# Performance work log

Hardware: AMD Instinct MI355X
Metric: run time of the kernel (lower is better)

Reference implementation:

```python
import jax, jax.numpy as jnp
import numpy as np

B, S, F, D, M = 2, 512, 16384, 768, 262144  # batch, seq, n_features, d_model, n_connections


def setup_inputs() -> dict:
    key = jax.random.key(0)
    k1, k2, k3, k4, k5 = jax.random.split(key, 5)
    up_facts = jax.random.normal(k1, (B, S, F), dtype=jnp.float32)
    down_encoder = jax.random.normal(k2, (F, D), dtype=jnp.float32) * 0.02
    up_decoder = jax.random.normal(k3, (D, F), dtype=jnp.float32) * 0.02
    i_indices = jnp.sort(jax.random.randint(k4, (M,), 0, F, dtype=jnp.int32)).astype(jnp.int64)
    j_indices = jax.random.randint(k5, (M,), 0, F, dtype=jnp.int32).astype(jnp.int64)
    return {
        "up_facts": up_facts,
        "down_encoder": down_encoder,
        "up_decoder": up_decoder,
        "i_indices": i_indices,
        "j_indices": j_indices,
    }


def reference(up_facts, down_encoder, up_decoder, i_indices, j_indices):
    # Virtual weight value for each sparse connection (i -> j):
    #   values[m] = <down_encoder[i_m, :], up_decoder[:, j_m]>
    values = jnp.sum(down_encoder[i_indices] * up_decoder[:, j_indices].T, axis=1)  # [M]
    # Gather upstream feature activations for each connection, scale by value.
    scaled = up_facts[:, :, j_indices] * values  # [B, S, M]
    # Scatter-add into downstream feature slots (duplicate i indices accumulate).
    contributions = jnp.zeros((up_facts.shape[0], up_facts.shape[1], down_encoder.shape[0]),
                              dtype=up_facts.dtype)
    return contributions.at[:, :, i_indices].add(scaled)  # [B, S, F]
```

## Files before the change

kernel.cpp:

```cpp
#include <hip/hip_runtime.h>
#include <hip/hip_bf16.h>

#define D_DIM 768
#define F_DIM 16384
#define M_CONN 262144
#define N_ROWS 1024

typedef float f32x4 __attribute__((ext_vector_type(4)));
typedef float f32x2 __attribute__((ext_vector_type(2)));

__device__ __forceinline__ float bf2f(unsigned short u) {
    return __uint_as_float(((unsigned int)u) << 16);
}

__global__ __launch_bounds__(512) void transpose_f32_t(const float* __restrict__ in,
                                                       float* __restrict__ out,
                                                       int R, int C) {
    __shared__ float ldsT[128][132];
    const int t = threadIdx.x;
    const int x0 = blockIdx.x * 128;
    const int y0 = blockIdx.y * 128;
#pragma unroll
    for (int it = 0; it < 8; ++it) {
        const int idx = it * 512 + t;
        const int r = idx >> 5;
        const int c4 = idx & 31;
        const f32x4 v = __builtin_nontemporal_load(
            (const f32x4*)(in + (size_t)(y0 + r) * C + x0 + c4 * 4));
        ldsT[c4 * 4 + 0][r] = v.x;
        ldsT[c4 * 4 + 1][r] = v.y;
        ldsT[c4 * 4 + 2][r] = v.z;
        ldsT[c4 * 4 + 3][r] = v.w;
    }
    __syncthreads();
#pragma unroll
    for (int it = 0; it < 8; ++it) {
        const int idx = it * 512 + t;
        const int c = idx >> 5;
        const int r4 = idx & 31;
        const f32x4 o = *(const f32x4*)&ldsT[c][r4 * 4];
        __builtin_nontemporal_store(
            o, (f32x4*)(out + (size_t)(x0 + c) * R + y0 + r4 * 4));
    }
}

__global__ __launch_bounds__(512) void transpose_f2b_t(const float* __restrict__ in,
                                                       unsigned short* __restrict__ out,
                                                       int R, int C) {
    __shared__ unsigned short ldsT[128][260];
    const int t = threadIdx.x;
    const int x0 = blockIdx.x * 128;
    const int y0 = blockIdx.y * 256;
#pragma unroll
    for (int it = 0; it < 16; ++it) {
        const int idx = it * 512 + t;
        const int r = idx >> 5;
        const int c4 = idx & 31;
        const f32x4 v = __builtin_nontemporal_load(
            (const f32x4*)(in + (size_t)(y0 + r) * C + x0 + c4 * 4));
        __hip_bfloat16 b0 = __float2bfloat16(v.x);
        __hip_bfloat16 b1 = __float2bfloat16(v.y);
        __hip_bfloat16 b2 = __float2bfloat16(v.z);
        __hip_bfloat16 b3 = __float2bfloat16(v.w);
        ldsT[c4 * 4 + 0][r] = *(unsigned short*)&b0;
        ldsT[c4 * 4 + 1][r] = *(unsigned short*)&b1;
        ldsT[c4 * 4 + 2][r] = *(unsigned short*)&b2;
        ldsT[c4 * 4 + 3][r] = *(unsigned short*)&b3;
    }
    __syncthreads();
#pragma unroll
    for (int it = 0; it < 16; ++it) {
        const int idx = it * 512 + t;
        const int c = idx >> 6;
        const int r4 = idx & 63;
        const ushort4 o = *(const ushort4*)&ldsT[c][r4 * 4];
        *(ushort4*)(out + (size_t)(x0 + c) * R + y0 + r4 * 4) = o;
    }
}

__global__ __launch_bounds__(256) void values_kernel(const float* __restrict__ de,
                                                     const unsigned short* __restrict__ udT,
                                                     const int* __restrict__ i_idx,
                                                     const int* __restrict__ j_idx,
                                                     float* __restrict__ values) {
    const int wave = (blockIdx.x * blockDim.x + threadIdx.x) >> 6;
    const int lane = threadIdx.x & 63;
    const int mbase = wave * 4;

    int ii[4], jj[4];
#pragma unroll
    for (int t = 0; t < 4; ++t) {
        ii[t] = i_idx[mbase + t];
        jj[t] = j_idx[mbase + t];
    }
    ushort4 u[4][3];
#pragma unroll
    for (int t = 0; t < 4; ++t) {
        const ushort4* b = (const ushort4*)(udT + (size_t)jj[t] * D_DIM);
        u[t][0] = b[lane]; u[t][1] = b[lane + 64]; u[t][2] = b[lane + 128];
    }

    int cur_i = -1;
    float4 a0, a1, a2;
#pragma unroll
    for (int t = 0; t < 4; ++t) {
        const int i = ii[t];
        if (i != cur_i) {
            const float4* a = (const float4*)(de + (size_t)i * D_DIM);
            a0 = a[lane]; a1 = a[lane + 64]; a2 = a[lane + 128];
            cur_i = i;
        }
        float s = 0.f;
        s = fmaf(a0.x, bf2f(u[t][0].x), s); s = fmaf(a0.y, bf2f(u[t][0].y), s);
        s = fmaf(a0.z, bf2f(u[t][0].z), s); s = fmaf(a0.w, bf2f(u[t][0].w), s);
        s = fmaf(a1.x, bf2f(u[t][1].x), s); s = fmaf(a1.y, bf2f(u[t][1].y), s);
        s = fmaf(a1.z, bf2f(u[t][1].z), s); s = fmaf(a1.w, bf2f(u[t][1].w), s);
        s = fmaf(a2.x, bf2f(u[t][2].x), s); s = fmaf(a2.y, bf2f(u[t][2].y), s);
        s = fmaf(a2.z, bf2f(u[t][2].z), s); s = fmaf(a2.w, bf2f(u[t][2].w), s);
#pragma unroll
        for (int off = 32; off > 0; off >>= 1)
            s += __shfl_down(s, off, 64);
        if (lane == 0) values[mbase + t] = s;
    }
}

__global__ __launch_bounds__(256) void seg_kernel(const int* __restrict__ i_idx,
                                                  int* __restrict__ seg) {
    const int i = blockIdx.x * blockDim.x + threadIdx.x;
    if (i > F_DIM) return;
    if (i == F_DIM) { seg[i] = M_CONN; return; }
    int lo = 0, hi = M_CONN;
    while (lo < hi) {
        int mid = (lo + hi) >> 1;
        if (i_idx[mid] < i) lo = mid + 1; else hi = mid;
    }
    seg[i] = lo;
}

__global__ __launch_bounds__(256) void spmm_tiled(const unsigned short* __restrict__ upT,
                                                  const int* __restrict__ j_idx,
                                                  const float* __restrict__ vals,
                                                  const int* __restrict__ seg,
                                                  float* __restrict__ outT) {
    const int i = blockIdx.x * 4 + (threadIdx.x >> 6);
    const int lane = threadIdx.x & 63;
    const int col0 = blockIdx.y * 128;
    const int ms = seg[i], me = seg[i + 1];

    f32x2 acc0 = {0.f, 0.f}, acc1 = {0.f, 0.f};
    f32x2 acc2 = {0.f, 0.f}, acc3 = {0.f, 0.f};
    int m = ms;
    for (; m + 3 < me; m += 4) {
        const int j0 = j_idx[m],     j1 = j_idx[m + 1];
        const int j2 = j_idx[m + 2], j3 = j_idx[m + 3];
        const float v0 = vals[m],     v1 = vals[m + 1];
        const float v2 = vals[m + 2], v3 = vals[m + 3];
        const unsigned int x0 = *(const unsigned int*)(upT + (size_t)j0 * N_ROWS + col0 + lane * 2);
        const unsigned int x1 = *(const unsigned int*)(upT + (size_t)j1 * N_ROWS + col0 + lane * 2);
        const unsigned int x2 = *(const unsigned int*)(upT + (size_t)j2 * N_ROWS + col0 + lane * 2);
        const unsigned int x3 = *(const unsigned int*)(upT + (size_t)j3 * N_ROWS + col0 + lane * 2);
        acc0.x = fmaf(v0, bf2f((unsigned short)(x0 & 0xffff)), acc0.x);
        acc0.y = fmaf(v0, bf2f((unsigned short)(x0 >> 16)),    acc0.y);
        acc1.x = fmaf(v1, bf2f((unsigned short)(x1 & 0xffff)), acc1.x);
        acc1.y = fmaf(v1, bf2f((unsigned short)(x1 >> 16)),    acc1.y);
        acc2.x = fmaf(v2, bf2f((unsigned short)(x2 & 0xffff)), acc2.x);
        acc2.y = fmaf(v2, bf2f((unsigned short)(x2 >> 16)),    acc2.y);
        acc3.x = fmaf(v3, bf2f((unsigned short)(x3 & 0xffff)), acc3.x);
        acc3.y = fmaf(v3, bf2f((unsigned short)(x3 >> 16)),    acc3.y);
    }
    for (; m < me; ++m) {
        const int j0 = j_idx[m];
        const float v0 = vals[m];
        const unsigned int x0 = *(const unsigned int*)(upT + (size_t)j0 * N_ROWS + col0 + lane * 2);
        acc0.x = fmaf(v0, bf2f((unsigned short)(x0 & 0xffff)), acc0.x);
        acc0.y = fmaf(v0, bf2f((unsigned short)(x0 >> 16)),    acc0.y);
    }
    f32x2 r;
    r.x = (acc0.x + acc1.x) + (acc2.x + acc3.x);
    r.y = (acc0.y + acc1.y) + (acc2.y + acc3.y);
    __builtin_nontemporal_store(r, (f32x2*)(outT + (size_t)i * N_ROWS + col0 + lane * 2));
}

extern "C" void kernel_launch(void* const* d_in, const int* in_sizes, int n_in,
                              void* d_out, int out_size, void* d_ws, size_t ws_size,
                              hipStream_t stream) {
    const float* up_facts = (const float*)d_in[0];
    const float* de       = (const float*)d_in[1];
    const float* ud       = (const float*)d_in[2];
    const int*   i_idx    = (const int*)d_in[3];
    const int*   j_idx    = (const int*)d_in[4];
    float* out = (float*)d_out;

    char* ws = (char*)d_ws;
    unsigned short* udT = (unsigned short*)ws;
    float* outT   = (float*)ws;
    float* values = (float*)(ws + (size_t)64 * 1024 * 1024);
    int*   seg    = (int*)  (ws + (size_t)65 * 1024 * 1024);
    unsigned short* upT = (unsigned short*)out;

    transpose_f2b_t<<<dim3(F_DIM / 128, D_DIM / 256), 512, 0, stream>>>(
        ud, udT, D_DIM, F_DIM);
    values_kernel<<<(M_CONN / 4) * 64 / 256, 256, 0, stream>>>(de, udT, i_idx, j_idx, values);
    transpose_f2b_t<<<dim3(F_DIM / 128, N_ROWS / 256), 512, 0, stream>>>(
        up_facts, upT, N_ROWS, F_DIM);
    seg_kernel<<<(F_DIM + 1 + 255) / 256, 256, 0, stream>>>(i_idx, seg);
    spmm_tiled<<<dim3(F_DIM / 4, 8), 256, 0, stream>>>(upT, j_idx, values, seg, outT);
    transpose_f32_t<<<dim3(N_ROWS / 128, F_DIM / 128), 512, 0, stream>>>(
        outT, out, F_DIM, N_ROWS);
}
```

Before: 349.2 us.

## Store SpMM output as bf16 and give each block one full output row

```diff
diff --git a/kernel.cpp b/kernel.cpp
--- a/kernel.cpp
+++ b/kernel.cpp
@@ -7,41 +7,10 @@
 #define N_ROWS 1024
 
 typedef float f32x4 __attribute__((ext_vector_type(4)));
-typedef float f32x2 __attribute__((ext_vector_type(2)));
+typedef unsigned short u16x4 __attribute__((ext_vector_type(4)));
 
 __device__ __forceinline__ float bf2f(unsigned short u) {
     return __uint_as_float(((unsigned int)u) << 16);
-}
-
-__global__ __launch_bounds__(512) void transpose_f32_t(const float* __restrict__ in,
-                                                       float* __restrict__ out,
-                                                       int R, int C) {
-    __shared__ float ldsT[128][132];
-    const int t = threadIdx.x;
-    const int x0 = blockIdx.x * 128;
-    const int y0 = blockIdx.y * 128;
-#pragma unroll
-    for (int it = 0; it < 8; ++it) {
-        const int idx = it * 512 + t;
-        const int r = idx >> 5;
-        const int c4 = idx & 31;
-        const f32x4 v = __builtin_nontemporal_load(
-            (const f32x4*)(in + (size_t)(y0 + r) * C + x0 + c4 * 4));
-        ldsT[c4 * 4 + 0][r] = v.x;
-        ldsT[c4 * 4 + 1][r] = v.y;
-        ldsT[c4 * 4 + 2][r] = v.z;
-        ldsT[c4 * 4 + 3][r] = v.w;
-    }
-    __syncthreads();
-#pragma unroll
-    for (int it = 0; it < 8; ++it) {
-        const int idx = it * 512 + t;
-        const int c = idx >> 5;
-        const int r4 = idx & 31;
-        const f32x4 o = *(const f32x4*)&ldsT[c][r4 * 4];
-        __builtin_nontemporal_store(
-            o, (f32x4*)(out + (size_t)(x0 + c) * R + y0 + r4 * 4));
-    }
 }
 
 __global__ __launch_bounds__(512) void transpose_f2b_t(const float* __restrict__ in,
@@ -73,8 +42,41 @@
         const int idx = it * 512 + t;
         const int c = idx >> 6;
         const int r4 = idx & 63;
-        const ushort4 o = *(const ushort4*)&ldsT[c][r4 * 4];
-        *(ushort4*)(out + (size_t)(x0 + c) * R + y0 + r4 * 4) = o;
+        const u16x4 o = *(const u16x4*)&ldsT[c][r4 * 4];
+        *(u16x4*)(out + (size_t)(x0 + c) * R + y0 + r4 * 4) = o;
+    }
+}
+
+__global__ __launch_bounds__(512) void transpose_b2f_t(const unsigned short* __restrict__ in,
+                                                       float* __restrict__ out,
+                                                       int R, int C) {
+    __shared__ unsigned short ldsT[256][130];
+    const int t = threadIdx.x;
+    const int x0 = blockIdx.x * 256;
+    const int y0 = blockIdx.y * 128;
+#pragma unroll
+    for (int it = 0; it < 16; ++it) {
+        const int idx = it * 512 + t;
+        const int r = idx >> 6;
+        const int c4 = idx & 63;
+        const u16x4 v = __builtin_nontemporal_load(
+            (const u16x4*)(in + (size_t)(y0 + r) * C + x0 + c4 * 4));
+        ldsT[c4 * 4 + 0][r] = v.x;
+        ldsT[c4 * 4 + 1][r] = v.y;
+        ldsT[c4 * 4 + 2][r] = v.z;
+        ldsT[c4 * 4 + 3][r] = v.w;
+    }
+    __syncthreads();
+#pragma unroll
+    for (int it = 0; it < 16; ++it) {
+        const int idx = it * 512 + t;
+        const int c = idx >> 5;
+        const int r4 = idx & 31;
+        const u16x4 o = *(const u16x4*)&ldsT[c][r4 * 4];
+        f32x4 f;
+        f.x = bf2f(o.x); f.y = bf2f(o.y); f.z = bf2f(o.z); f.w = bf2f(o.w);
+        __builtin_nontemporal_store(
+            f, (f32x4*)(out + (size_t)(x0 + c) * R + y0 + r4 * 4));
     }
 }
 
@@ -137,48 +139,58 @@
     seg[i] = lo;
 }
 
-__global__ __launch_bounds__(256) void spmm_tiled(const unsigned short* __restrict__ upT,
-                                                  const int* __restrict__ j_idx,
-                                                  const float* __restrict__ vals,
-                                                  const int* __restrict__ seg,
-                                                  float* __restrict__ outT) {
-    const int i = blockIdx.x * 4 + (threadIdx.x >> 6);
-    const int lane = threadIdx.x & 63;
-    const int col0 = blockIdx.y * 128;
+__global__ __launch_bounds__(256) void spmm_kernel(const unsigned short* __restrict__ upT,
+                                                   const int* __restrict__ j_idx,
+                                                   const float* __restrict__ vals,
+                                                   const int* __restrict__ seg,
+                                                   unsigned short* __restrict__ outT) {
+    const int i = blockIdx.x;
+    const int t = threadIdx.x;
     const int ms = seg[i], me = seg[i + 1];
-
-    f32x2 acc0 = {0.f, 0.f}, acc1 = {0.f, 0.f};
-    f32x2 acc2 = {0.f, 0.f}, acc3 = {0.f, 0.f};
+    float4 acc0 = make_float4(0.f, 0.f, 0.f, 0.f);
+    float4 acc1 = make_float4(0.f, 0.f, 0.f, 0.f);
+    float4 acc2 = make_float4(0.f, 0.f, 0.f, 0.f);
+    float4 acc3 = make_float4(0.f, 0.f, 0.f, 0.f);
     int m = ms;
     for (; m + 3 < me; m += 4) {
         const int j0 = j_idx[m],     j1 = j_idx[m + 1];
         const int j2 = j_idx[m + 2], j3 = j_idx[m + 3];
         const float v0 = vals[m],     v1 = vals[m + 1];
         const float v2 = vals[m + 2], v3 = vals[m + 3];
-        const unsigned int x0 = *(const unsigned int*)(upT + (size_t)j0 * N_ROWS + col0 + lane * 2);
-        const unsigned int x1 = *(const unsigned int*)(upT + (size_t)j1 * N_ROWS + col0 + lane * 2);
-        const unsigned int x2 = *(const unsigned int*)(upT + (size_t)j2 * N_ROWS + col0 + lane * 2);
-        const unsigned int x3 = *(const unsigned int*)(upT + (size_t)j3 * N_ROWS + col0 + lane * 2);
-        acc0.x = fmaf(v0, bf2f((unsigned short)(x0 & 0xffff)), acc0.x);
-        acc0.y = fmaf(v0, bf2f((unsigned short)(x0 >> 16)),    acc0.y);
-        acc1.x = fmaf(v1, bf2f((unsigned short)(x1 & 0xffff)), acc1.x);
-        acc1.y = fmaf(v1, bf2f((unsigned short)(x1 >> 16)),    acc1.y);
-        acc2.x = fmaf(v2, bf2f((unsigned short)(x2 & 0xffff)), acc2.x);
-        acc2.y = fmaf(v2, bf2f((unsigned short)(x2 >> 16)),    acc2.y);
-        acc3.x = fmaf(v3, bf2f((unsigned short)(x3 & 0xffff)), acc3.x);
-        acc3.y = fmaf(v3, bf2f((unsigned short)(x3 >> 16)),    acc3.y);
+        const ushort4 x0 = ((const ushort4*)(upT + (size_t)j0 * N_ROWS))[t];
+        const ushort4 x1 = ((const ushort4*)(upT + (size_t)j1 * N_ROWS))[t];
+        const ushort4 x2 = ((const ushort4*)(upT + (size_t)j2 * N_ROWS))[t];
+        const ushort4 x3 = ((const ushort4*)(upT + (size_t)j3 * N_ROWS))[t];
+        acc0.x = fmaf(v0, bf2f(x0.x), acc0.x); acc0.y = fmaf(v0, bf2f(x0.y), acc0.y);
+        acc0.z = fmaf(v0, bf2f(x0.z), acc0.z); acc0.w = fmaf(v0, bf2f(x0.w), acc0.w);
+        acc1.x = fmaf(v1, bf2f(x1.x), acc1.x); acc1.y = fmaf(v1, bf2f(x1.y), acc1.y);
+        acc1.z = fmaf(v1, bf2f(x1.z), acc1.z); acc1.w = fmaf(v1, bf2f(x1.w), acc1.w);
+        acc2.x = fmaf(v2, bf2f(x2.x), acc2.x); acc2.y = fmaf(v2, bf2f(x2.y), acc2.y);
+        acc2.z = fmaf(v2, bf2f(x2.z), acc2.z); acc2.w = fmaf(v2, bf2f(x2.w), acc2.w);
+        acc3.x = fmaf(v3, bf2f(x3.x), acc3.x); acc3.y = fmaf(v3, bf2f(x3.y), acc3.y);
+        acc3.z = fmaf(v3, bf2f(x3.z), acc3.z); acc3.w = fmaf(v3, bf2f(x3.w), acc3.w);
     }
     for (; m < me; ++m) {
         const int j0 = j_idx[m];
         const float v0 = vals[m];
-        const unsigned int x0 = *(const unsigned int*)(upT + (size_t)j0 * N_ROWS + col0 + lane * 2);
-        acc0.x = fmaf(v0, bf2f((unsigned short)(x0 & 0xffff)), acc0.x);
-        acc0.y = fmaf(v0, bf2f((unsigned short)(x0 >> 16)),    acc0.y);
-    }
-    f32x2 r;
-    r.x = (acc0.x + acc1.x) + (acc2.x + acc3.x);
-    r.y = (acc0.y + acc1.y) + (acc2.y + acc3.y);
-    __builtin_nontemporal_store(r, (f32x2*)(outT + (size_t)i * N_ROWS + col0 + lane * 2));
+        const ushort4 x0 = ((const ushort4*)(upT + (size_t)j0 * N_ROWS))[t];
+        acc0.x = fmaf(v0, bf2f(x0.x), acc0.x); acc0.y = fmaf(v0, bf2f(x0.y), acc0.y);
+        acc0.z = fmaf(v0, bf2f(x0.z), acc0.z); acc0.w = fmaf(v0, bf2f(x0.w), acc0.w);
+    }
+    const float rx = (acc0.x + acc1.x) + (acc2.x + acc3.x);
+    const float ry = (acc0.y + acc1.y) + (acc2.y + acc3.y);
+    const float rz = (acc0.z + acc1.z) + (acc2.z + acc3.z);
+    const float rw = (acc0.w + acc1.w) + (acc2.w + acc3.w);
+    __hip_bfloat16 b0 = __float2bfloat16(rx);
+    __hip_bfloat16 b1 = __float2bfloat16(ry);
+    __hip_bfloat16 b2 = __float2bfloat16(rz);
+    __hip_bfloat16 b3 = __float2bfloat16(rw);
+    u16x4 o;
+    o.x = *(unsigned short*)&b0;
+    o.y = *(unsigned short*)&b1;
+    o.z = *(unsigned short*)&b2;
+    o.w = *(unsigned short*)&b3;
+    __builtin_nontemporal_store(o, (u16x4*)(outT + (size_t)i * N_ROWS) + t);
 }
 
 extern "C" void kernel_launch(void* const* d_in, const int* in_sizes, int n_in,
@@ -192,8 +204,8 @@
     float* out = (float*)d_out;
 
     char* ws = (char*)d_ws;
-    unsigned short* udT = (unsigned short*)ws;
-    float* outT   = (float*)ws;
+    unsigned short* udT  = (unsigned short*)ws;
+    unsigned short* outT = (unsigned short*)(ws + (size_t)24 * 1024 * 1024);
     float* values = (float*)(ws + (size_t)64 * 1024 * 1024);
     int*   seg    = (int*)  (ws + (size_t)65 * 1024 * 1024);
     unsigned short* upT = (unsigned short*)out;
@@ -204,7 +216,7 @@
     transpose_f2b_t<<<dim3(F_DIM / 128, N_ROWS / 256), 512, 0, stream>>>(
         up_facts, upT, N_ROWS, F_DIM);
     seg_kernel<<<(F_DIM + 1 + 255) / 256, 256, 0, stream>>>(i_idx, seg);
-    spmm_tiled<<<dim3(F_DIM / 4, 8), 256, 0, stream>>>(upT, j_idx, values, seg, outT);
-    transpose_f32_t<<<dim3(N_ROWS / 128, F_DIM / 128), 512, 0, stream>>>(
+    spmm_kernel<<<F_DIM, 256, 0, stream>>>(upT, j_idx, values, seg, outT);
+    transpose_b2f_t<<<dim3(N_ROWS / 256, F_DIM / 128), 512, 0, stream>>>(
         outT, out, F_DIM, N_ROWS);
 }
```

Result: faster. 328.5 us (-5.9%).
